# Kernel optimization log

Hardware: AMD Instinct MI355X
Metric: run time of the kernel (lower is better)

## Reference

```python
import jax, jax.numpy as jnp
import numpy as np

DIM = 2048
N_HEADS = 32
N_KV_HEADS = 8
HEAD_DIM = DIM // N_HEADS  # 64
N_REP = N_HEADS // N_KV_HEADS  # 4
B, S = 1, 2048


def _rope(t, cos, sin):
    # t: (b, s, h, head_dim); cos/sin: (s, head_dim//2)
    tr = t.reshape(*t.shape[:-1], -1, 2)
    a, b = tr[..., 0], tr[..., 1]
    c = cos[None, :, None, :]
    s_ = sin[None, :, None, :]
    ra = a * c - b * s_
    rb = a * s_ + b * c
    return jnp.stack([ra, rb], axis=-1).reshape(t.shape)


def setup_inputs() -> dict:
    key = jax.random.key(0)
    ks = jax.random.split(key, 6)
    sc = 1.0 / np.sqrt(DIM)
    x = jax.random.normal(ks[0], (B, S, DIM), dtype=jnp.float32)
    wq = jax.random.normal(ks[1], (DIM, N_HEADS * HEAD_DIM), dtype=jnp.float32) * sc
    wk = jax.random.normal(ks[2], (DIM, N_KV_HEADS * HEAD_DIM), dtype=jnp.float32) * sc
    wv = jax.random.normal(ks[3], (DIM, N_KV_HEADS * HEAD_DIM), dtype=jnp.float32) * sc
    wo = jax.random.normal(ks[4], (N_HEADS * HEAD_DIM, DIM), dtype=jnp.float32) * sc
    # rotary frequencies (theta = 500000 as in Llama3)
    inv = 1.0 / (500000.0 ** (np.arange(0, HEAD_DIM, 2, dtype=np.float32) / HEAD_DIM))
    ang = np.arange(S, dtype=np.float32)[:, None] * inv[None, :]
    freqs_cos = jnp.asarray(np.cos(ang), dtype=jnp.float32)
    freqs_sin = jnp.asarray(np.sin(ang), dtype=jnp.float32)
    # causal additive mask
    mask = jnp.triu(jnp.full((S, S), -1e9, dtype=jnp.float32), k=1)
    return {"x": x, "wq": wq, "wk": wk, "wv": wv, "wo": wo,
            "freqs_cos": freqs_cos, "freqs_sin": freqs_sin, "mask": mask,
            "start_pos": 0}


def reference(x, wq, wk, wv, wo, freqs_cos, freqs_sin, mask, start_pos):
    b, s, _ = x.shape
    xq = (x @ wq).reshape(b, s, N_HEADS, HEAD_DIM)
    xk = (x @ wk).reshape(b, s, N_KV_HEADS, HEAD_DIM)
    xv = (x @ wv).reshape(b, s, N_KV_HEADS, HEAD_DIM)
    xq = _rope(xq, freqs_cos, freqs_sin)
    xk = _rope(xk, freqs_cos, freqs_sin)
    # GQA without repeat_interleave: view queries as (b, s, kv, rep, d)
    q = xq.reshape(b, s, N_KV_HEADS, N_REP, HEAD_DIM)
    scale = 1.0 / np.sqrt(HEAD_DIM)
    # scores: (b, kv, rep, q, k)
    scores = jnp.einsum('bqkrd,bskd->bkrqs', q, xk) * scale
    scores = scores + mask[None, None, None, :, :]
    probs = jax.nn.softmax(scores.astype(jnp.float32), axis=-1).astype(x.dtype)
    out = jnp.einsum('bkrqs,bskd->bqkrd', probs, xv)
    out = out.reshape(b, s, N_HEADS * HEAD_DIM)
    return out @ wo
```

## Files before the change

kernel.cpp:

```cpp
#include <hip/hip_runtime.h>
#include <hip/hip_bf16.h>

#define DIM 2048
#define S_LEN 2048
#define N_HEADS 32
#define N_KV_HEADS 8
#define HEAD_DIM 64
#define KV_DIM (N_KV_HEADS * HEAD_DIM)
#define QKV_N (DIM + 2 * KV_DIM)
#define QSCALE 0.18033688011112042f

typedef __attribute__((ext_vector_type(8))) short bf16x8;
typedef __attribute__((ext_vector_type(4))) float f32x4;

__device__ __forceinline__ unsigned short bf16_of(float f) {
    __hip_bfloat16 h = __float2bfloat16(f);
    return *reinterpret_cast<unsigned short*>(&h);
}
__device__ __forceinline__ float f_of_bf16(unsigned short u) {
    unsigned int x = ((unsigned int)u) << 16;
    return __uint_as_float(x);
}
__device__ __forceinline__ void gl_lds16(const void* g, void* l) {
    __builtin_amdgcn_global_load_lds((const __attribute__((address_space(1))) void*)g,
                                     (__attribute__((address_space(3))) void*)l, 16, 0, 0);
}
__device__ __forceinline__ unsigned int pack2bf(float a, float b) {
    return (unsigned int)bf16_of(a) | ((unsigned int)bf16_of(b) << 16);
}

__global__ __launch_bounds__(256) void prep(const float* __restrict__ x,
                                            const float* __restrict__ wq,
                                            const float* __restrict__ wk,
                                            const float* __restrict__ wv,
                                            const float* __restrict__ wo,
                                            unsigned short* __restrict__ xbf,
                                            unsigned short* __restrict__ wqkvT,
                                            unsigned short* __restrict__ woT) {
    __shared__ float tile[64][65];
    const int t = threadIdx.x;
    int b = blockIdx.x;
    if (b < 4096) {
        int idx = b * 256 + t;
        float4 f = ((const float4*)x)[idx];
        ushort4 u;
        u.x = bf16_of(f.x); u.y = bf16_of(f.y); u.z = bf16_of(f.z); u.w = bf16_of(f.w);
        ((ushort4*)xbf)[idx] = u;
        return;
    }
    b -= 4096;
    const float* src;
    unsigned short* dst;
    int src_cols, bx, by;
    if (b < 1024)      { src = wq; dst = wqkvT;                                src_cols = DIM;    bx = b & 31;          by = b >> 5; }
    else if (b < 1280) { src = wk; dst = wqkvT + (size_t)DIM * DIM;            src_cols = KV_DIM; bx = (b - 1024) & 7;  by = (b - 1024) >> 3; }
    else if (b < 1536) { src = wv; dst = wqkvT + (size_t)(DIM + KV_DIM) * DIM; src_cols = KV_DIM; bx = (b - 1280) & 7;  by = (b - 1280) >> 3; }
    else               { src = wo; dst = woT;                                  src_cols = DIM;    bx = (b - 1536) & 31; by = (b - 1536) >> 5; }
    const int c0 = bx * 64, r0 = by * 64;
#pragma unroll
    for (int i = 0; i < 16; i++) {
        int idx = t + i * 256;
        int r = idx >> 6, c = idx & 63;
        tile[r][c] = src[(size_t)(r0 + r) * src_cols + c0 + c];
    }
    __syncthreads();
#pragma unroll
    for (int i = 0; i < 16; i++) {
        int idx = t + i * 256;
        int r = idx >> 6, c = idx & 63;
        dst[(size_t)(c0 + r) * DIM + r0 + c] = bf16_of(tile[c][r]);
    }
}

__global__ __launch_bounds__(256) void gemm_bt64(const unsigned short* __restrict__ A,
                                                 const unsigned short* __restrict__ Bt,
                                                 void* __restrict__ Cv,
                                                 int M, int N, int K, int c_bf16) {
    __shared__ unsigned short As[128 * 64];
    __shared__ unsigned short Bs[64 * 64];
    const int tid = threadIdx.x;
    const int wave = tid >> 6, lane = tid & 63;
    const int m16 = lane & 15, quad = lane >> 4;
    const int m0 = blockIdx.y * 128, n0 = blockIdx.x * 64;
    const int wm = (wave >> 1) * 64, wn = (wave & 1) * 32;

    const int lrow = lane >> 3;
    const int gc = (lane & 7) ^ lrow;
    const unsigned short* Ab = A + (size_t)(m0 + wave * 8 + lrow) * K + gc * 8;
    const unsigned short* Bb = Bt + (size_t)(n0 + wave * 8 + lrow) * K + gc * 8;

    f32x4 acc[4][2];
#pragma unroll
    for (int mb = 0; mb < 4; mb++)
#pragma unroll
        for (int nb = 0; nb < 2; nb++) acc[mb][nb] = (f32x4){0.f, 0.f, 0.f, 0.f};

    for (int k0 = 0; k0 < K; k0 += 64) {
#pragma unroll
        for (int g = 0; g < 4; g++)
            gl_lds16(Ab + (size_t)g * 32 * K + k0, &As[(g * 32 + wave * 8) * 64]);
#pragma unroll
        for (int g = 0; g < 2; g++)
            gl_lds16(Bb + (size_t)g * 32 * K + k0, &Bs[(g * 32 + wave * 8) * 64]);
        __syncthreads();
#pragma unroll
        for (int ks = 0; ks < 2; ks++) {
            const int ch = (ks * 4 + quad) ^ (m16 & 7);
            bf16x8 af[4], bfr[2];
#pragma unroll
            for (int mb = 0; mb < 4; mb++)
                af[mb] = *(const bf16x8*)&As[(wm + mb * 16 + m16) * 64 + ch * 8];
#pragma unroll
            for (int nb = 0; nb < 2; nb++)
                bfr[nb] = *(const bf16x8*)&Bs[(wn + nb * 16 + m16) * 64 + ch * 8];
#pragma unroll
            for (int mb = 0; mb < 4; mb++)
#pragma unroll
                for (int nb = 0; nb < 2; nb++)
                    acc[mb][nb] = __builtin_amdgcn_mfma_f32_16x16x32_bf16(af[mb], bfr[nb], acc[mb][nb], 0, 0, 0);
        }
        __syncthreads();
    }

    if (c_bf16) {
        unsigned short* C = (unsigned short*)Cv;
#pragma unroll
        for (int mb = 0; mb < 4; mb++)
#pragma unroll
            for (int nb = 0; nb < 2; nb++)
#pragma unroll
                for (int r = 0; r < 4; r++)
                    C[(size_t)(m0 + wm + mb * 16 + quad * 4 + r) * N + n0 + wn + nb * 16 + m16] =
                        bf16_of(acc[mb][nb][r]);
    } else {
        float* C = (float*)Cv;
#pragma unroll
        for (int mb = 0; mb < 4; mb++)
#pragma unroll
            for (int nb = 0; nb < 2; nb++)
#pragma unroll
                for (int r = 0; r < 4; r++)
                    C[(size_t)(m0 + wm + mb * 16 + quad * 4 + r) * N + n0 + wn + nb * 16 + m16] =
                        acc[mb][nb][r];
    }
}

__global__ __launch_bounds__(256) void rope_tv(const unsigned short* __restrict__ qkv,
                                               unsigned short* __restrict__ qbf,
                                               unsigned short* __restrict__ kbf,
                                               unsigned short* __restrict__ vbt,
                                               const float* __restrict__ fcos,
                                               const float* __restrict__ fsin) {
    __shared__ unsigned short tile[64][65];
    const int t = threadIdx.x;
    int b = blockIdx.x;
    if (b < 2560) {
        int idx = b * 256 + t;
        const int nq = S_LEN * N_HEADS * 8;
        int s, j, srcoff, dstoff;
        unsigned short* dst;
        float osc;
        if (idx < nq) {
            s = idx >> 8;
            int rem = idx & 255;
            int h = rem >> 3;
            j = rem & 7;
            srcoff = s * QKV_N + h * 64 + j * 8;
            dstoff = s * DIM + h * 64 + j * 8;
            dst = qbf;
            osc = QSCALE;
        } else {
            int t2 = idx - nq;
            s = t2 >> 6;
            int rem = t2 & 63;
            int h = rem >> 3;
            j = rem & 7;
            srcoff = s * QKV_N + DIM + h * 64 + j * 8;
            dstoff = s * KV_DIM + h * 64 + j * 8;
            dst = kbf;
            osc = 1.0f;
        }
        bf16x8 v8 = *(const bf16x8*)&qkv[srcoff];
        float4 c4 = *(const float4*)&fcos[s * 32 + j * 4];
        float4 s4 = *(const float4*)&fsin[s * 32 + j * 4];
        float cs[4] = {c4.x, c4.y, c4.z, c4.w};
        float sn[4] = {s4.x, s4.y, s4.z, s4.w};
        bf16x8 o;
#pragma unroll
        for (int p = 0; p < 4; p++) {
            float a = f_of_bf16((unsigned short)v8[2 * p]);
            float bb = f_of_bf16((unsigned short)v8[2 * p + 1]);
            o[2 * p]     = (short)bf16_of((a * cs[p] - bb * sn[p]) * osc);
            o[2 * p + 1] = (short)bf16_of((a * sn[p] + bb * cs[p]) * osc);
        }
        *(bf16x8*)&dst[dstoff] = o;
        return;
    }
    b -= 2560;
    const int d0 = (b & 7) * 64;
    const int s0 = (b >> 3) * 64;
#pragma unroll
    for (int i = 0; i < 16; i++) {
        int idx = t + i * 256;
        int r = idx >> 6, c = idx & 63;
        tile[r][c] = qkv[(size_t)(s0 + r) * QKV_N + DIM + KV_DIM + d0 + c];
    }
    __syncthreads();
#pragma unroll
    for (int i = 0; i < 16; i++) {
        int idx = t + i * 256;
        int r = idx >> 6, c = idx & 63;
        int key = s0 + c;
        int kl = key & 127;
        int kp = (kl & 0x60) | ((kl & 0x0C) << 1) | ((kl & 0x10) >> 2) | (kl & 3);
        vbt[(size_t)(d0 + r) * S_LEN + (key & ~127) + kp] = tile[c][r];
    }
}

__global__ __launch_bounds__(256) void attn_mfma4(const unsigned short* __restrict__ qb,
                                                  const unsigned short* __restrict__ kb,
                                                  const unsigned short* __restrict__ vbt,
                                                  unsigned short* __restrict__ O0,
                                                  unsigned short* __restrict__ O1,
                                                  float2* __restrict__ ml0,
                                                  float2* __restrict__ ml1) {
    const int bx   = blockIdx.x;
    const int part = blockIdx.y;
    const int h    = blockIdx.z;
    const int kh = h >> 2;
    const int tid  = threadIdx.x;
    const int wave = tid >> 6;
    const int lane = tid & 63;
    const int m16  = lane & 15;
    const int quad = lane >> 4;

    unsigned short* Op = part ? O1 : O0;
    float2* mlp = part ? ml1 : ml0;

    __shared__ unsigned short Ks[128 * 64];
    __shared__ unsigned short Vt[64 * 128];

    const int lrow8 = lane >> 3;
    const int kc    = (lane & 7) ^ lrow8;
    const int lrow4 = lane >> 4;
    const int vc    = (lane & 15) ^ ((wave * 4 + lrow4) & 7);

    const unsigned short* Kbase = kb + (size_t)kh * 64 + (size_t)(wave * 8 + lrow8) * KV_DIM + kc * 8;
    const unsigned short* Vbase = vbt + (size_t)(kh * 64 + wave * 4 + lrow4) * S_LEN + vc * 8;

#pragma unroll
    for (int half = 0; half < 2; half++) {
        const int qt = half ? bx : (31 - bx);
        const int q0 = qt * 64;
        const int n_full = (qt >> 1) + 1;
        const int n0 = (n_full + 1) >> 1;
        const int kt_lo = part ? n0 : 0;
        const int kt_hi = part ? n_full : n0;

        bf16x8 qa[2];
        {
            const int qrow = q0 + wave * 16 + m16;
#pragma unroll
            for (int ks = 0; ks < 2; ks++)
                qa[ks] = *(const bf16x8*)&qb[(size_t)qrow * DIM + h * 64 + ks * 32 + quad * 8];
        }

        f32x4 o_acc[4];
#pragma unroll
        for (int nb = 0; nb < 4; nb++) o_acc[nb] = (f32x4){0.f, 0.f, 0.f, 0.f};
        float m_s = -1e30f, l_s = 0.f;
        const int qrow_lane = q0 + wave * 16 + m16;
        const int orow_base = q0 + wave * 16 + quad * 4;

        for (int kt = kt_lo; kt < kt_hi; kt++) {
#pragma unroll
            for (int g = 0; g < 4; g++) {
                gl_lds16(Kbase + (size_t)(kt * 128 + g * 32) * KV_DIM, &Ks[(g * 32 + wave * 8) * 64]);
                gl_lds16(Vbase + (size_t)g * 16 * S_LEN + kt * 128, &Vt[(g * 16 + wave * 4) * 128]);
            }
            __syncthreads();

            f32x4 sc[8];
#pragma unroll
            for (int cb = 0; cb < 8; cb++) sc[cb] = (f32x4){0.f, 0.f, 0.f, 0.f};
#pragma unroll
            for (int ks = 0; ks < 2; ks++) {
                const int slot = (ks * 4 + quad) ^ (m16 & 7);
#pragma unroll
                for (int cb = 0; cb < 8; cb++) {
                    bf16x8 kf = *(const bf16x8*)&Ks[(cb * 16 + m16) * 64 + slot * 8];
                    sc[cb] = __builtin_amdgcn_mfma_f32_16x16x32_bf16(kf, qa[ks], sc[cb], 0, 0, 0);
                }
            }

            if (kt == n_full - 1) {
#pragma unroll
                for (int cb = 0; cb < 8; cb++) {
                    int key = kt * 128 + cb * 16 + quad * 4;
#pragma unroll
                    for (int r = 0; r < 4; r++)
                        if (key + r > qrow_lane) sc[cb][r] = -1e30f;
                }
            }

            float rmax = sc[0][0];
#pragma unroll
            for (int cb = 0; cb < 8; cb++)
#pragma unroll
                for (int r = 0; r < 4; r++) rmax = fmaxf(rmax, sc[cb][r]);
            rmax = fmaxf(rmax, __shfl_xor(rmax, 16, 64));
            rmax = fmaxf(rmax, __shfl_xor(rmax, 32, 64));

            float mnew = fmaxf(m_s, rmax);
            float alpha = __builtin_amdgcn_exp2f(m_s - mnew);
            m_s = mnew;

            float rsum = 0.f;
#pragma unroll
            for (int cb = 0; cb < 8; cb++)
#pragma unroll
                for (int r = 0; r < 4; r++) {
                    float p = __builtin_amdgcn_exp2f(sc[cb][r] - mnew);
                    sc[cb][r] = p;
                    rsum += p;
                }
            rsum += __shfl_xor(rsum, 16, 64);
            rsum += __shfl_xor(rsum, 32, 64);
            l_s = l_s * alpha + rsum;

            unsigned int P01[8], P23[8];
#pragma unroll
            for (int cb = 0; cb < 8; cb++) {
                P01[cb] = pack2bf(sc[cb][0], sc[cb][1]);
                P23[cb] = pack2bf(sc[cb][2], sc[cb][3]);
            }

#pragma unroll
            for (int r = 0; r < 4; r++) {
                float a_r = __shfl(alpha, quad * 4 + r, 64);
#pragma unroll
                for (int nb = 0; nb < 4; nb++) o_acc[nb][r] *= a_r;
            }

#pragma unroll
            for (int ks = 0; ks < 4; ks++) {
                union { unsigned int u[4]; bf16x8 v; } pa;
                pa.u[0] = P01[2 * ks];     pa.u[1] = P23[2 * ks];
                pa.u[2] = P01[2 * ks + 1]; pa.u[3] = P23[2 * ks + 1];
                const int slot = (ks * 4 + quad) ^ (m16 & 7);
#pragma unroll
                for (int nb = 0; nb < 4; nb++) {
                    bf16x8 vf = *(const bf16x8*)&Vt[(nb * 16 + m16) * 128 + slot * 8];
                    o_acc[nb] = __builtin_amdgcn_mfma_f32_16x16x32_bf16(pa.v, vf, o_acc[nb], 0, 0, 0);
                }
            }
            __syncthreads();
        }

#pragma unroll
        for (int r = 0; r < 4; r++) {
            float l_r = __shfl(l_s, quad * 4 + r, 64);
            float inv_l = (l_r > 0.f) ? (1.f / l_r) : 0.f;
#pragma unroll
            for (int nb = 0; nb < 4; nb++)
                Op[(size_t)(orow_base + r) * DIM + h * 64 + nb * 16 + m16] =
                    bf16_of(o_acc[nb][r] * inv_l);
        }
        if (quad == 0)
            mlp[h * S_LEN + q0 + wave * 16 + m16] = make_float2(m_s, l_s);
    }
}

__global__ __launch_bounds__(256) void combine(unsigned short* __restrict__ O0,
                                               const unsigned short* __restrict__ O1,
                                               const float2* __restrict__ ml0,
                                               const float2* __restrict__ ml1) {
    int idx = blockIdx.x * 256 + threadIdx.x;
    int row = idx >> 9;
    int cc = (idx & 511) * 4;
    int h = cc >> 6;
    float2 a0 = ml0[h * S_LEN + row];
    float2 a1 = ml1[h * S_LEN + row];
    float m = fmaxf(a0.x, a1.x);
    float w0 = a0.y * __builtin_amdgcn_exp2f(a0.x - m);
    float w1 = a1.y * __builtin_amdgcn_exp2f(a1.x - m);
    float inv = 1.f / (w0 + w1);
    w0 *= inv; w1 *= inv;
    ushort4 u0 = *(const ushort4*)&O0[(size_t)row * DIM + cc];
    ushort4 u1 = *(const ushort4*)&O1[(size_t)row * DIM + cc];
    ushort4 o;
    o.x = bf16_of(w0 * f_of_bf16(u0.x) + w1 * f_of_bf16(u1.x));
    o.y = bf16_of(w0 * f_of_bf16(u0.y) + w1 * f_of_bf16(u1.y));
    o.z = bf16_of(w0 * f_of_bf16(u0.z) + w1 * f_of_bf16(u1.z));
    o.w = bf16_of(w0 * f_of_bf16(u0.w) + w1 * f_of_bf16(u1.w));
    *(ushort4*)&O0[(size_t)row * DIM + cc] = o;
}

extern "C" void kernel_launch(void* const* d_in, const int* in_sizes, int n_in,
                              void* d_out, int out_size, void* d_ws, size_t ws_size,
                              hipStream_t stream) {
    const float* x    = (const float*)d_in[0];
    const float* wq   = (const float*)d_in[1];
    const float* wk   = (const float*)d_in[2];
    const float* wv   = (const float*)d_in[3];
    const float* wo   = (const float*)d_in[4];
    const float* fcos = (const float*)d_in[5];
    const float* fsin = (const float*)d_in[6];

    char* ws = (char*)d_ws;
    const size_t MB = 1024 * 1024;
    unsigned short* xbf    = (unsigned short*)(ws);
    unsigned short* wqkvT  = (unsigned short*)(ws + 8 * MB);
    unsigned short* woT    = (unsigned short*)(ws + 20 * MB);
    unsigned short* qkvbf  = (unsigned short*)(ws + 28 * MB);
    unsigned short* vbt    = (unsigned short*)(ws + 40 * MB);
    float2*         ml0    = (float2*)(ws + 42 * MB);
    float2*         ml1    = (float2*)(ws + 42 * MB + 512 * 1024);
    unsigned short* qbf    = (unsigned short*)(ws + 8 * MB);
    unsigned short* kbf    = (unsigned short*)(ws + 16 * MB);
    unsigned short* Opart0 = (unsigned short*)(ws);
    unsigned short* Opart1 = (unsigned short*)(ws + 28 * MB);

    prep<<<4096 + 2560, 256, 0, stream>>>(x, wq, wk, wv, wo, xbf, wqkvT, woT);

    gemm_bt64<<<dim3(QKV_N / 64, S_LEN / 128), 256, 0, stream>>>(xbf, wqkvT, qkvbf,
                                                                 S_LEN, QKV_N, DIM, 1);

    rope_tv<<<2560 + 256, 256, 0, stream>>>(qkvbf, qbf, kbf, vbt, fcos, fsin);

    attn_mfma4<<<dim3(16, 2, N_HEADS), 256, 0, stream>>>(qbf, kbf, vbt,
                                                         Opart0, Opart1, ml0, ml1);

    combine<<<(S_LEN * DIM / 4) / 256, 256, 0, stream>>>(Opart0, Opart1, ml0, ml1);

    gemm_bt64<<<dim3(DIM / 64, S_LEN / 128), 256, 0, stream>>>(Opart0, woT, d_out,
                                                               S_LEN, DIM, DIM, 0);
}
```

Measured before the change: 238.7 us.

## Drop split-K attention and combine; double-buffer K/V tiles and sum rows via MFMA

Each attention block now walks the full causal key range for its query tiles, so the two-part split and the separate combine kernel go away. K/V tiles are double-buffered in LDS, so the next tile's global-to-LDS load overlaps the current tile's compute. This also removes the trailing barrier. The row sum is computed by an MFMA against a ones vector instead of shuffles, and the bf16 packing becomes a truncating byte permute. In exchange the grid has half as many blocks, which lowers parallelism, and truncation in place of rounding slightly changes numerics.

```diff
diff --git a/kernel.cpp b/kernel.cpp
--- a/kernel.cpp
+++ b/kernel.cpp
@@ -25,8 +25,8 @@
     __builtin_amdgcn_global_load_lds((const __attribute__((address_space(1))) void*)g,
                                      (__attribute__((address_space(3))) void*)l, 16, 0, 0);
 }
-__device__ __forceinline__ unsigned int pack2bf(float a, float b) {
-    return (unsigned int)bf16_of(a) | ((unsigned int)bf16_of(b) << 16);
+__device__ __forceinline__ unsigned int pack2tr(float lo, float hi) {
+    return __builtin_amdgcn_perm(__float_as_uint(hi), __float_as_uint(lo), 0x07060302u);
 }
 
 __global__ __launch_bounds__(256) void prep(const float* __restrict__ x,
@@ -217,16 +217,12 @@
     }
 }
 
-__global__ __launch_bounds__(256) void attn_mfma4(const unsigned short* __restrict__ qb,
+__global__ __launch_bounds__(256) void attn_mfma5(const unsigned short* __restrict__ qb,
                                                   const unsigned short* __restrict__ kb,
                                                   const unsigned short* __restrict__ vbt,
-                                                  unsigned short* __restrict__ O0,
-                                                  unsigned short* __restrict__ O1,
-                                                  float2* __restrict__ ml0,
-                                                  float2* __restrict__ ml1) {
-    const int bx   = blockIdx.x;
-    const int part = blockIdx.y;
-    const int h    = blockIdx.z;
+                                                  unsigned short* __restrict__ out) {
+    const int h  = blockIdx.y;
+    const int bx = blockIdx.x;
     const int kh = h >> 2;
     const int tid  = threadIdx.x;
     const int wave = tid >> 6;
@@ -234,11 +230,8 @@
     const int m16  = lane & 15;
     const int quad = lane >> 4;
 
-    unsigned short* Op = part ? O1 : O0;
-    float2* mlp = part ? ml1 : ml0;
-
-    __shared__ unsigned short Ks[128 * 64];
-    __shared__ unsigned short Vt[64 * 128];
+    __shared__ unsigned short Ks[2][128 * 64];
+    __shared__ unsigned short Vt[2][64 * 128];
 
     const int lrow8 = lane >> 3;
     const int kc    = (lane & 7) ^ lrow8;
@@ -248,14 +241,15 @@
     const unsigned short* Kbase = kb + (size_t)kh * 64 + (size_t)(wave * 8 + lrow8) * KV_DIM + kc * 8;
     const unsigned short* Vbase = vbt + (size_t)(kh * 64 + wave * 4 + lrow4) * S_LEN + vc * 8;
 
+    bf16x8 ones;
+#pragma unroll
+    for (int i = 0; i < 8; i++) ones[i] = (short)0x3F80;
+
 #pragma unroll
     for (int half = 0; half < 2; half++) {
         const int qt = half ? bx : (31 - bx);
         const int q0 = qt * 64;
-        const int n_full = (qt >> 1) + 1;
-        const int n0 = (n_full + 1) >> 1;
-        const int kt_lo = part ? n0 : 0;
-        const int kt_hi = part ? n_full : n0;
+        const int n_iter = (qt >> 1) + 1;
 
         bf16x8 qa[2];
         {
@@ -268,17 +262,33 @@
         f32x4 o_acc[4];
 #pragma unroll
         for (int nb = 0; nb < 4; nb++) o_acc[nb] = (f32x4){0.f, 0.f, 0.f, 0.f};
-        float m_s = -1e30f, l_s = 0.f;
+        f32x4 l_acc = (f32x4){0.f, 0.f, 0.f, 0.f};
+        float m_s = -1e30f;
         const int qrow_lane = q0 + wave * 16 + m16;
         const int orow_base = q0 + wave * 16 + quad * 4;
 
-        for (int kt = kt_lo; kt < kt_hi; kt++) {
-#pragma unroll
-            for (int g = 0; g < 4; g++) {
-                gl_lds16(Kbase + (size_t)(kt * 128 + g * 32) * KV_DIM, &Ks[(g * 32 + wave * 8) * 64]);
-                gl_lds16(Vbase + (size_t)g * 16 * S_LEN + kt * 128, &Vt[(g * 16 + wave * 4) * 128]);
-            }
+        if (half) __syncthreads();
+
+#pragma unroll
+        for (int g = 0; g < 4; g++) {
+            gl_lds16(Kbase + (size_t)(g * 32) * KV_DIM, &Ks[0][(g * 32 + wave * 8) * 64]);
+            gl_lds16(Vbase + (size_t)g * 16 * S_LEN, &Vt[0][(g * 16 + wave * 4) * 128]);
+        }
+
+        for (int kt = 0; kt < n_iter; kt++) {
             __syncthreads();
+            if (kt + 1 < n_iter) {
+                const int nb2 = (kt + 1) & 1;
+#pragma unroll
+                for (int g = 0; g < 4; g++) {
+                    gl_lds16(Kbase + (size_t)((kt + 1) * 128 + g * 32) * KV_DIM,
+                             &Ks[nb2][(g * 32 + wave * 8) * 64]);
+                    gl_lds16(Vbase + (size_t)g * 16 * S_LEN + (kt + 1) * 128,
+                             &Vt[nb2][(g * 16 + wave * 4) * 128]);
+                }
+            }
+            const unsigned short* K_ = Ks[kt & 1];
+            const unsigned short* V_ = Vt[kt & 1];
 
             f32x4 sc[8];
 #pragma unroll
@@ -288,12 +298,12 @@
                 const int slot = (ks * 4 + quad) ^ (m16 & 7);
 #pragma unroll
                 for (int cb = 0; cb < 8; cb++) {
-                    bf16x8 kf = *(const bf16x8*)&Ks[(cb * 16 + m16) * 64 + slot * 8];
+                    bf16x8 kf = *(const bf16x8*)&K_[(cb * 16 + m16) * 64 + slot * 8];
                     sc[cb] = __builtin_amdgcn_mfma_f32_16x16x32_bf16(kf, qa[ks], sc[cb], 0, 0, 0);
                 }
             }
 
-            if (kt == n_full - 1) {
+            if (kt == n_iter - 1) {
 #pragma unroll
                 for (int cb = 0; cb < 8; cb++) {
                     int key = kt * 128 + cb * 16 + quad * 4;
@@ -303,11 +313,12 @@
                 }
             }
 
-            float rmax = sc[0][0];
-#pragma unroll
-            for (int cb = 0; cb < 8; cb++)
-#pragma unroll
-                for (int r = 0; r < 4; r++) rmax = fmaxf(rmax, sc[cb][r]);
+            float rmax = fmaxf(fmaxf(sc[0][0], sc[0][1]), fmaxf(sc[0][2], sc[0][3]));
+#pragma unroll
+            for (int cb = 1; cb < 8; cb++) {
+                float c1 = fmaxf(fmaxf(sc[cb][0], sc[cb][1]), fmaxf(sc[cb][2], sc[cb][3]));
+                rmax = fmaxf(rmax, c1);
+            }
             rmax = fmaxf(rmax, __shfl_xor(rmax, 16, 64));
             rmax = fmaxf(rmax, __shfl_xor(rmax, 32, 64));
 
@@ -315,24 +326,17 @@
             float alpha = __builtin_amdgcn_exp2f(m_s - mnew);
             m_s = mnew;
 
-            float rsum = 0.f;
 #pragma unroll
             for (int cb = 0; cb < 8; cb++)
 #pragma unroll
-                for (int r = 0; r < 4; r++) {
-                    float p = __builtin_amdgcn_exp2f(sc[cb][r] - mnew);
-                    sc[cb][r] = p;
-                    rsum += p;
-                }
-            rsum += __shfl_xor(rsum, 16, 64);
-            rsum += __shfl_xor(rsum, 32, 64);
-            l_s = l_s * alpha + rsum;
+                for (int r = 0; r < 4; r++)
+                    sc[cb][r] = __builtin_amdgcn_exp2f(sc[cb][r] - mnew);
 
             unsigned int P01[8], P23[8];
 #pragma unroll
             for (int cb = 0; cb < 8; cb++) {
-                P01[cb] = pack2bf(sc[cb][0], sc[cb][1]);
-                P23[cb] = pack2bf(sc[cb][2], sc[cb][3]);
+                P01[cb] = pack2tr(sc[cb][0], sc[cb][1]);
+                P23[cb] = pack2tr(sc[cb][2], sc[cb][3]);
             }
 
 #pragma unroll
@@ -340,6 +344,7 @@
                 float a_r = __shfl(alpha, quad * 4 + r, 64);
 #pragma unroll
                 for (int nb = 0; nb < 4; nb++) o_acc[nb][r] *= a_r;
+                l_acc[r] *= a_r;
             }
 
 #pragma unroll
@@ -350,50 +355,22 @@
                 const int slot = (ks * 4 + quad) ^ (m16 & 7);
 #pragma unroll
                 for (int nb = 0; nb < 4; nb++) {
-                    bf16x8 vf = *(const bf16x8*)&Vt[(nb * 16 + m16) * 128 + slot * 8];
+                    bf16x8 vf = *(const bf16x8*)&V_[(nb * 16 + m16) * 128 + slot * 8];
                     o_acc[nb] = __builtin_amdgcn_mfma_f32_16x16x32_bf16(pa.v, vf, o_acc[nb], 0, 0, 0);
                 }
-            }
-            __syncthreads();
+                l_acc = __builtin_amdgcn_mfma_f32_16x16x32_bf16(pa.v, ones, l_acc, 0, 0, 0);
+            }
         }
 
 #pragma unroll
         for (int r = 0; r < 4; r++) {
-            float l_r = __shfl(l_s, quad * 4 + r, 64);
-            float inv_l = (l_r > 0.f) ? (1.f / l_r) : 0.f;
+            float inv_l = 1.f / l_acc[r];
 #pragma unroll
             for (int nb = 0; nb < 4; nb++)
-                Op[(size_t)(orow_base + r) * DIM + h * 64 + nb * 16 + m16] =
+                out[(size_t)(orow_base + r) * DIM + h * 64 + nb * 16 + m16] =
                     bf16_of(o_acc[nb][r] * inv_l);
         }
-        if (quad == 0)
-            mlp[h * S_LEN + q0 + wave * 16 + m16] = make_float2(m_s, l_s);
-    }
-}
-
-__global__ __launch_bounds__(256) void combine(unsigned short* __restrict__ O0,
-                                               const unsigned short* __restrict__ O1,
-                                               const float2* __restrict__ ml0,
-                                               const float2* __restrict__ ml1) {
-    int idx = blockIdx.x * 256 + threadIdx.x;
-    int row = idx >> 9;
-    int cc = (idx & 511) * 4;
-    int h = cc >> 6;
-    float2 a0 = ml0[h * S_LEN + row];
-    float2 a1 = ml1[h * S_LEN + row];
-    float m = fmaxf(a0.x, a1.x);
-    float w0 = a0.y * __builtin_amdgcn_exp2f(a0.x - m);
-    float w1 = a1.y * __builtin_amdgcn_exp2f(a1.x - m);
-    float inv = 1.f / (w0 + w1);
-    w0 *= inv; w1 *= inv;
-    ushort4 u0 = *(const ushort4*)&O0[(size_t)row * DIM + cc];
-    ushort4 u1 = *(const ushort4*)&O1[(size_t)row * DIM + cc];
-    ushort4 o;
-    o.x = bf16_of(w0 * f_of_bf16(u0.x) + w1 * f_of_bf16(u1.x));
-    o.y = bf16_of(w0 * f_of_bf16(u0.y) + w1 * f_of_bf16(u1.y));
-    o.z = bf16_of(w0 * f_of_bf16(u0.z) + w1 * f_of_bf16(u1.z));
-    o.w = bf16_of(w0 * f_of_bf16(u0.w) + w1 * f_of_bf16(u1.w));
-    *(ushort4*)&O0[(size_t)row * DIM + cc] = o;
+    }
 }
 
 extern "C" void kernel_launch(void* const* d_in, const int* in_sizes, int n_in,
@@ -414,12 +391,9 @@
     unsigned short* woT    = (unsigned short*)(ws + 20 * MB);
     unsigned short* qkvbf  = (unsigned short*)(ws + 28 * MB);
     unsigned short* vbt    = (unsigned short*)(ws + 40 * MB);
-    float2*         ml0    = (float2*)(ws + 42 * MB);
-    float2*         ml1    = (float2*)(ws + 42 * MB + 512 * 1024);
     unsigned short* qbf    = (unsigned short*)(ws + 8 * MB);
     unsigned short* kbf    = (unsigned short*)(ws + 16 * MB);
-    unsigned short* Opart0 = (unsigned short*)(ws);
-    unsigned short* Opart1 = (unsigned short*)(ws + 28 * MB);
+    unsigned short* attnbf = (unsigned short*)(ws);
 
     prep<<<4096 + 2560, 256, 0, stream>>>(x, wq, wk, wv, wo, xbf, wqkvT, woT);
 
@@ -428,11 +402,8 @@
 
     rope_tv<<<2560 + 256, 256, 0, stream>>>(qkvbf, qbf, kbf, vbt, fcos, fsin);
 
-    attn_mfma4<<<dim3(16, 2, N_HEADS), 256, 0, stream>>>(qbf, kbf, vbt,
-                                                         Opart0, Opart1, ml0, ml1);
-
-    combine<<<(S_LEN * DIM / 4) / 256, 256, 0, stream>>>(Opart0, Opart1, ml0, ml1);
-
-    gemm_bt64<<<dim3(DIM / 64, S_LEN / 128), 256, 0, stream>>>(Opart0, woT, d_out,
+    attn_mfma5<<<dim3(16, N_HEADS), 256, 0, stream>>>(qbf, kbf, vbt, attnbf);
+
+    gemm_bt64<<<dim3(DIM / 64, S_LEN / 128), 256, 0, stream>>>(attnbf, woT, d_out,
                                                                S_LEN, DIM, DIM, 0);
 }
```

Measured after the change: 227.7 us. -4.6%, faster.
